# Kernel optimization log

Measured on AMD Instinct MI355X. Metric: run time of the kernel, lower is better.

Reference implementation:

```python
import jax, jax.numpy as jnp
import numpy as np

IN_FEATURES = 4096
OUT_FEATURES = 16384
BATCH = 2
SEQ = 2048


def setup_inputs() -> dict:
    key = jax.random.key(0)
    k_x, k_s, k_sgn, k_b = jax.random.split(key, 4)
    x = jax.random.normal(k_x, (BATCH, SEQ, IN_FEATURES), dtype=jnp.float32)
    # stored: uint8-style inverse-log magnitudes in [1, 255]
    stored = jax.random.randint(k_s, (OUT_FEATURES, IN_FEATURES), 1, 256, dtype=jnp.int32)
    # sign in {0,1}; mapped to {-1,+1} inside reference
    sign = jax.random.randint(k_sgn, (OUT_FEATURES, IN_FEATURES), 0, 2, dtype=jnp.int32)
    # log range matching typical weight magnitudes exp(-8)..exp(0)
    log_min = jnp.full((1,), -8.0, dtype=jnp.float32)
    log_max = jnp.full((1,), 0.0, dtype=jnp.float32)
    bias = jax.random.normal(k_b, (OUT_FEATURES,), dtype=jnp.float32) * 0.02
    return {"x": x, "stored": stored, "sign": sign, "log_min": log_min,
            "log_max": log_max, "bias": bias}


def _dequant_qins(stored, sign, log_min, log_max):
    # reverse inverse mapping: stored in [1,255] -> normalized in [0,1]
    normalized = (255.0 - stored.astype(jnp.float32)) / 254.0
    log_weight = log_min + normalized * (log_max - log_min)
    sign_f = (2 * sign - 1).astype(jnp.float32)  # {0,1} -> {-1,+1}
    return sign_f * jnp.exp(log_weight)  # [out, in] fp32


def reference(x, stored, sign, log_min, log_max, bias):
    lmin = log_min[0]
    lmax = log_max[0]
    w = _dequant_qins(stored, sign, lmin, lmax)  # [O, I]
    # F.linear: y = x @ w.T + bias
    out = jnp.einsum('bsi,oi->bso', x, w) + bias
    return out
```

## Files before the change

### kernel.cpp

```cpp
#include <hip/hip_runtime.h>
#include <stdint.h>

#define M_DIM 4096
#define N_DIM 16384
#define K_DIM 4096
#define BM 256
#define BN 256
#define BK 64
#define NT (K_DIM / BK)

typedef __attribute__((ext_vector_type(8))) __bf16 bf16x8;
typedef __attribute__((ext_vector_type(4))) float f32x4;

__device__ __forceinline__ unsigned short f2bf(float f) {
    uint32_t u = __builtin_bit_cast(uint32_t, f);
    uint32_t r = (u + 0x7FFFu + ((u >> 16) & 1u)) >> 16;
    return (unsigned short)r;
}

union Pack8 { unsigned short h[8]; uint4 v; };

__device__ __forceinline__ void async_copy16(const void* g, void* l) {
    __builtin_amdgcn_global_load_lds((__attribute__((address_space(1))) void*)(g),
                                     (__attribute__((address_space(3))) void*)(l),
                                     16, 0, 0);
}

#define BARRIER() do { asm volatile("" ::: "memory"); \
                       __builtin_amdgcn_s_barrier();  \
                       asm volatile("" ::: "memory"); } while (0)

__global__ __launch_bounds__(256) void cast_x_kernel(const float* __restrict__ x,
                                                     unsigned short* __restrict__ xb,
                                                     int n8) {
    for (int i = blockIdx.x * blockDim.x + threadIdx.x; i < n8;
         i += gridDim.x * blockDim.x) {
        const float4* p = (const float4*)(x + (size_t)i * 8);
        float4 v0 = p[0], v1 = p[1];
        Pack8 o;
        o.h[0] = f2bf(v0.x); o.h[1] = f2bf(v0.y);
        o.h[2] = f2bf(v0.z); o.h[3] = f2bf(v0.w);
        o.h[4] = f2bf(v1.x); o.h[5] = f2bf(v1.y);
        o.h[6] = f2bf(v1.z); o.h[7] = f2bf(v1.w);
        *(uint4*)(xb + (size_t)i * 8) = o.v;
    }
}

__global__ __launch_bounds__(256) void dequant_kernel(const int* __restrict__ stored,
                                                      const int* __restrict__ sign,
                                                      const float* __restrict__ log_min,
                                                      const float* __restrict__ log_max,
                                                      unsigned short* __restrict__ wb,
                                                      int n8) {
    const float lmin = log_min[0];
    const float lrange = log_max[0] - lmin;
    for (int i = blockIdx.x * blockDim.x + threadIdx.x; i < n8;
         i += gridDim.x * blockDim.x) {
        const int4* ps = (const int4*)(stored + (size_t)i * 8);
        const int4* pg = (const int4*)(sign + (size_t)i * 8);
        int4 s0 = ps[0], s1 = ps[1];
        int4 g0 = pg[0], g1 = pg[1];
        int sv[8] = {s0.x, s0.y, s0.z, s0.w, s1.x, s1.y, s1.z, s1.w};
        int gv[8] = {g0.x, g0.y, g0.z, g0.w, g1.x, g1.y, g1.z, g1.w};
        Pack8 o;
#pragma unroll
        for (int j = 0; j < 8; ++j) {
            float nrm = (255.0f - (float)sv[j]) * (1.0f / 254.0f);
            float w = __expf(lmin + nrm * lrange);
            o.h[j] = f2bf(gv[j] ? w : -w);
        }
        *(uint4*)(wb + (size_t)i * 8) = o.v;
    }
}

__global__ __launch_bounds__(512, 1) void gemm_kernel(const unsigned short* __restrict__ A,
                                                      const unsigned short* __restrict__ W,
                                                      const float* __restrict__ bias,
                                                      float* __restrict__ C) {
    extern __shared__ char lds[];
    const int tid  = threadIdx.x;
    const int wave = tid >> 6;
    const int lane = tid & 63;
    const int l15  = lane & 15;
    const int l16  = lane >> 4;
    const int wr   = wave >> 2;
    const int wc   = wave & 3;

    const int bid = blockIdx.x;
    const int wg  = ((bid & 7) << 7) | (bid >> 3);
    const int rowBase = (wg >> 6) * BM;
    const int colBase = (wg & 63) * BN;

    f32x4 acc[8][4] = {};

    auto stage_half = [&](int t, int d, int u) {
        const int kb = t * BK;
        const unsigned short* g = (u < 2) ? A : W;
        const int rb = ((u < 2) ? rowBase : colBase) + (u & 1) * 128;
        char* hb = lds + d * 65536 + ((u < 2) ? 0 : 32768) + (u & 1) * 16384;
#pragma unroll
        for (int sub = 0; sub < 2; ++sub) {
            const int Ld   = (sub * 512 + tid) * 16;
            const int r    = Ld >> 7;
            const int colb = (Ld & 127) ^ ((r & 7) << 4);
            async_copy16(g + (size_t)(rb + r) * K_DIM + kb + (colb >> 1),
                         hb + (sub * 512 + wave * 64) * 16);
        }
    };

    stage_half(0, 0, 0); stage_half(0, 0, 1);
    stage_half(0, 0, 2); stage_half(0, 0, 3);
    stage_half(1, 1, 0); stage_half(1, 1, 1);

    for (int t = 0; t < NT; ++t) {
        const int c = t & 1;
        if (t + 1 < NT) asm volatile("s_waitcnt vmcnt(4)" ::: "memory");
        else            asm volatile("s_waitcnt vmcnt(0)" ::: "memory");
        BARRIER();
        __builtin_amdgcn_sched_barrier(0);

        const char* bA  = lds + c * 65536 + wr * 16384;
        const char* bB  = lds + c * 65536 + 32768 + (wc >> 1) * 16384;
        const int   brB = (wc & 1) * 64;

        bf16x8 aF[4][2];
        bf16x8 bF[2][2];
#pragma unroll
        for (int q = 0; q < 4; ++q) {
            const int mq = q >> 1, nq = q & 1;
            if (nq == 0) {
#pragma unroll
                for (int i = 0; i < 4; ++i)
#pragma unroll
                    for (int ks = 0; ks < 2; ++ks) {
                        const int r    = (mq * 4 + i) * 16 + l15;
                        const int colb = (ks * 64 + l16 * 16) ^ ((r & 7) << 4);
                        aF[i][ks] = *(const bf16x8*)(bA + (r << 7) + colb);
                    }
            }
#pragma unroll
            for (int j = 0; j < 2; ++j)
#pragma unroll
                for (int ks = 0; ks < 2; ++ks) {
                    const int r    = brB + (nq * 2 + j) * 16 + l15;
                    const int colb = (ks * 64 + l16 * 16) ^ ((r & 7) << 4);
                    bF[j][ks] = *(const bf16x8*)(bB + (r << 7) + colb);
                }
            if (q == 0 && t + 1 < NT) stage_half(t + 1, c ^ 1, 2);
            if (q == 1 && t + 1 < NT) stage_half(t + 1, c ^ 1, 3);
            if (q == 3 && t + 2 < NT) {
                stage_half(t + 2, c, 0);
                stage_half(t + 2, c, 1);
            }
            BARRIER();
            asm volatile("s_waitcnt lgkmcnt(0)" ::: "memory");
            __builtin_amdgcn_sched_barrier(0);
            __builtin_amdgcn_s_setprio(1);
#pragma unroll
            for (int i = 0; i < 4; ++i)
#pragma unroll
                for (int j = 0; j < 2; ++j)
#pragma unroll
                    for (int ks = 0; ks < 2; ++ks)
                        acc[mq * 4 + i][nq * 2 + j] =
                            __builtin_amdgcn_mfma_f32_16x16x32_bf16(
                                aF[i][ks], bF[j][ks], acc[mq * 4 + i][nq * 2 + j],
                                0, 0, 0);
            __builtin_amdgcn_s_setprio(0);
            BARRIER();
        }
    }

#pragma unroll
    for (int m = 0; m < 8; ++m) {
        const int grow0 = rowBase + wr * 128 + m * 16 + l16 * 4;
#pragma unroll
        for (int n = 0; n < 4; ++n) {
            const int gcol = colBase + wc * 64 + n * 16 + l15;
            const float bv = bias[gcol];
#pragma unroll
            for (int r4 = 0; r4 < 4; ++r4)
                C[(size_t)(grow0 + r4) * N_DIM + gcol] = acc[m][n][r4] + bv;
        }
    }
}

extern "C" void kernel_launch(void* const* d_in, const int* in_sizes, int n_in,
                              void* d_out, int out_size, void* d_ws, size_t ws_size,
                              hipStream_t stream) {
    const float* x       = (const float*)d_in[0];
    const int*   stored  = (const int*)d_in[1];
    const int*   sign    = (const int*)d_in[2];
    const float* log_min = (const float*)d_in[3];
    const float* log_max = (const float*)d_in[4];
    const float* bias    = (const float*)d_in[5];
    float* out = (float*)d_out;

    unsigned short* Ab = (unsigned short*)d_ws;
    unsigned short* Wb = (unsigned short*)((char*)d_ws +
                          (size_t)M_DIM * K_DIM * sizeof(unsigned short));

    cast_x_kernel<<<2048, 256, 0, stream>>>(x, Ab, (M_DIM * K_DIM) / 8);
    dequant_kernel<<<4096, 256, 0, stream>>>(stored, sign, log_min, log_max, Wb,
                                             (N_DIM * K_DIM) / 8);

    hipFuncSetAttribute((const void*)gemm_kernel,
                        hipFuncAttributeMaxDynamicSharedMemorySize, 131072);
    gemm_kernel<<<dim3((M_DIM / BM) * (N_DIM / BN)), dim3(512), 131072, stream>>>(
        Ab, Wb, bias, out);
}
```

Measured before the change: 654.1 us.

## Shrink GEMM tiles to 128x128 with simpler double-buffered pipeline

Halves the block tile from 256x256 to 128x128, so there are four times as many workgroups, with 64 KB of LDS each. The launch bound now asks for four blocks per CU instead of one. The staged quarter-pipeline is replaced by a plain double buffer: the next K tile is prefetched once per iteration and each wave computes a 64x32 sub-tile. The aim is more occupancy and simpler synchronisation. The cost is less operand reuse per loaded byte, a higher ratio of LDS reads to MFMAs, and more global and L2 traffic.

```diff
diff --git a/kernel.cpp b/kernel.cpp
--- a/kernel.cpp
+++ b/kernel.cpp
@@ -4,8 +4,8 @@
 #define M_DIM 4096
 #define N_DIM 16384
 #define K_DIM 4096
-#define BM 256
-#define BN 256
+#define BM 128
+#define BN 128
 #define BK 64
 #define NT (K_DIM / BK)
 
@@ -73,7 +73,7 @@
     }
 }
 
-__global__ __launch_bounds__(512, 1) void gemm_kernel(const unsigned short* __restrict__ A,
+__global__ __launch_bounds__(512, 4) void gemm_kernel(const unsigned short* __restrict__ A,
                                                       const unsigned short* __restrict__ W,
                                                       const float* __restrict__ bias,
                                                       float* __restrict__ C) {
@@ -87,17 +87,17 @@
     const int wc   = wave & 3;
 
     const int bid = blockIdx.x;
-    const int wg  = ((bid & 7) << 7) | (bid >> 3);
-    const int rowBase = (wg >> 6) * BM;
-    const int colBase = (wg & 63) * BN;
+    const int wg  = ((bid & 7) << 9) | (bid >> 3);
+    const int rowBase = (wg >> 7) * BM;
+    const int colBase = (wg & 127) * BN;
 
-    f32x4 acc[8][4] = {};
+    f32x4 acc[4][2] = {};
 
-    auto stage_half = [&](int t, int d, int u) {
+    auto stage = [&](int t, int u) {
         const int kb = t * BK;
-        const unsigned short* g = (u < 2) ? A : W;
-        const int rb = ((u < 2) ? rowBase : colBase) + (u & 1) * 128;
-        char* hb = lds + d * 65536 + ((u < 2) ? 0 : 32768) + (u & 1) * 16384;
+        const unsigned short* g = u ? W : A;
+        const int rb = u ? colBase : rowBase;
+        char* hb = lds + ((t & 1) << 15) + (u << 14);
 #pragma unroll
         for (int sub = 0; sub < 2; ++sub) {
             const int Ld   = (sub * 512 + tid) * 16;
@@ -108,75 +108,63 @@
         }
     };
 
-    stage_half(0, 0, 0); stage_half(0, 0, 1);
-    stage_half(0, 0, 2); stage_half(0, 0, 3);
-    stage_half(1, 1, 0); stage_half(1, 1, 1);
+    stage(0, 0); stage(0, 1);
 
     for (int t = 0; t < NT; ++t) {
         const int c = t & 1;
-        if (t + 1 < NT) asm volatile("s_waitcnt vmcnt(4)" ::: "memory");
-        else            asm volatile("s_waitcnt vmcnt(0)" ::: "memory");
+        if (t + 1 < NT) {
+            stage(t + 1, 0);
+            asm volatile("s_waitcnt vmcnt(2)" ::: "memory");
+        } else {
+            asm volatile("s_waitcnt vmcnt(0)" ::: "memory");
+        }
         BARRIER();
         __builtin_amdgcn_sched_barrier(0);
 
-        const char* bA  = lds + c * 65536 + wr * 16384;
-        const char* bB  = lds + c * 65536 + 32768 + (wc >> 1) * 16384;
-        const int   brB = (wc & 1) * 64;
+        const char* bA = lds + (c << 15);
+        const char* bB = lds + (c << 15) + 16384;
 
-        bf16x8 aF[4][2];
-        bf16x8 bF[2][2];
+        bf16x8 aF[4][2], bF[2][2];
 #pragma unroll
-        for (int q = 0; q < 4; ++q) {
-            const int mq = q >> 1, nq = q & 1;
-            if (nq == 0) {
+        for (int m = 0; m < 4; ++m)
 #pragma unroll
-                for (int i = 0; i < 4; ++i)
-#pragma unroll
-                    for (int ks = 0; ks < 2; ++ks) {
-                        const int r    = (mq * 4 + i) * 16 + l15;
-                        const int colb = (ks * 64 + l16 * 16) ^ ((r & 7) << 4);
-                        aF[i][ks] = *(const bf16x8*)(bA + (r << 7) + colb);
-                    }
+            for (int ks = 0; ks < 2; ++ks) {
+                const int r    = wr * 64 + m * 16 + l15;
+                const int colb = (ks * 64 + l16 * 16) ^ ((r & 7) << 4);
+                aF[m][ks] = *(const bf16x8*)(bA + (r << 7) + colb);
             }
 #pragma unroll
-            for (int j = 0; j < 2; ++j)
+        for (int n = 0; n < 2; ++n)
 #pragma unroll
-                for (int ks = 0; ks < 2; ++ks) {
-                    const int r    = brB + (nq * 2 + j) * 16 + l15;
-                    const int colb = (ks * 64 + l16 * 16) ^ ((r & 7) << 4);
-                    bF[j][ks] = *(const bf16x8*)(bB + (r << 7) + colb);
-                }
-            if (q == 0 && t + 1 < NT) stage_half(t + 1, c ^ 1, 2);
-            if (q == 1 && t + 1 < NT) stage_half(t + 1, c ^ 1, 3);
-            if (q == 3 && t + 2 < NT) {
-                stage_half(t + 2, c, 0);
-                stage_half(t + 2, c, 1);
+            for (int ks = 0; ks < 2; ++ks) {
+                const int r    = wc * 32 + n * 16 + l15;
+                const int colb = (ks * 64 + l16 * 16) ^ ((r & 7) << 4);
+                bF[n][ks] = *(const bf16x8*)(bB + (r << 7) + colb);
             }
-            BARRIER();
-            asm volatile("s_waitcnt lgkmcnt(0)" ::: "memory");
-            __builtin_amdgcn_sched_barrier(0);
-            __builtin_amdgcn_s_setprio(1);
+        if (t + 1 < NT) stage(t + 1, 1);
+        asm volatile("s_waitcnt lgkmcnt(8)" ::: "memory");
+        BARRIER();
+        asm volatile("s_waitcnt lgkmcnt(0)" ::: "memory");
+        __builtin_amdgcn_sched_barrier(0);
+        __builtin_amdgcn_s_setprio(1);
 #pragma unroll
-            for (int i = 0; i < 4; ++i)
+        for (int m = 0; m < 4; ++m)
 #pragma unroll
-                for (int j = 0; j < 2; ++j)
+            for (int n = 0; n < 2; ++n)
 #pragma unroll
-                    for (int ks = 0; ks < 2; ++ks)
-                        acc[mq * 4 + i][nq * 2 + j] =
-                            __builtin_amdgcn_mfma_f32_16x16x32_bf16(
-                                aF[i][ks], bF[j][ks], acc[mq * 4 + i][nq * 2 + j],
-                                0, 0, 0);
-            __builtin_amdgcn_s_setprio(0);
-            BARRIER();
-        }
+                for (int ks = 0; ks < 2; ++ks)
+                    acc[m][n] = __builtin_amdgcn_mfma_f32_16x16x32_bf16(
+                        aF[m][ks], bF[n][ks], acc[m][n], 0, 0, 0);
+        __builtin_amdgcn_s_setprio(0);
+        BARRIER();
     }
 
 #pragma unroll
-    for (int m = 0; m < 8; ++m) {
-        const int grow0 = rowBase + wr * 128 + m * 16 + l16 * 4;
+    for (int m = 0; m < 4; ++m) {
+        const int grow0 = rowBase + wr * 64 + m * 16 + l16 * 4;
 #pragma unroll
-        for (int n = 0; n < 4; ++n) {
-            const int gcol = colBase + wc * 64 + n * 16 + l15;
+        for (int n = 0; n < 2; ++n) {
+            const int gcol = colBase + wc * 32 + n * 16 + l15;
             const float bv = bias[gcol];
 #pragma unroll
             for (int r4 = 0; r4 < 4; ++r4)
@@ -205,7 +193,7 @@
                                              (N_DIM * K_DIM) / 8);
 
     hipFuncSetAttribute((const void*)gemm_kernel,
-                        hipFuncAttributeMaxDynamicSharedMemorySize, 131072);
-    gemm_kernel<<<dim3((M_DIM / BM) * (N_DIM / BN)), dim3(512), 131072, stream>>>(
+                        hipFuncAttributeMaxDynamicSharedMemorySize, 65536);
+    gemm_kernel<<<dim3((M_DIM / BM) * (N_DIM / BN)), dim3(512), 65536, stream>>>(
         Ab, Wb, bias, out);
 }
```

Result: slower. 783.1 us (+19.7%).

## Restructure GEMM main loop into four MFMA phases with fewer barriers

Applied to the files above, without the earlier changes.

Replaces the four-quadrant inner loop, which used two barriers per quadrant, with a flatter schedule. Both B fragment halves and the first A half are loaded up front, the second A half is loaded mid-iteration, and only one barrier remains before the t+2 prefetch. Global-to-LDS prefetches are interleaved between the MFMA blocks to cut synchronisation overhead. It also raises launch bounds to request two blocks per CU. That caps registers well below what the 128 accumulators plus all live A/B fragments need, so spills are a serious risk, and the 128 KB LDS allocation may not allow a second block anyway.

```diff
diff --git a/kernel.cpp b/kernel.cpp
--- a/kernel.cpp
+++ b/kernel.cpp
@@ -73,7 +73,7 @@
     }
 }
 
-__global__ __launch_bounds__(512, 1) void gemm_kernel(const unsigned short* __restrict__ A,
+__global__ __launch_bounds__(512, 2) void gemm_kernel(const unsigned short* __restrict__ A,
                                                       const unsigned short* __restrict__ W,
                                                       const float* __restrict__ bias,
                                                       float* __restrict__ C) {
@@ -117,58 +117,92 @@
         if (t + 1 < NT) asm volatile("s_waitcnt vmcnt(4)" ::: "memory");
         else            asm volatile("s_waitcnt vmcnt(0)" ::: "memory");
         BARRIER();
-        __builtin_amdgcn_sched_barrier(0);
 
         const char* bA  = lds + c * 65536 + wr * 16384;
         const char* bB  = lds + c * 65536 + 32768 + (wc >> 1) * 16384;
         const int   brB = (wc & 1) * 64;
 
-        bf16x8 aF[4][2];
-        bf16x8 bF[2][2];
-#pragma unroll
-        for (int q = 0; q < 4; ++q) {
-            const int mq = q >> 1, nq = q & 1;
-            if (nq == 0) {
-#pragma unroll
-                for (int i = 0; i < 4; ++i)
-#pragma unroll
-                    for (int ks = 0; ks < 2; ++ks) {
-                        const int r    = (mq * 4 + i) * 16 + l15;
-                        const int colb = (ks * 64 + l16 * 16) ^ ((r & 7) << 4);
-                        aF[i][ks] = *(const bf16x8*)(bA + (r << 7) + colb);
-                    }
-            }
-#pragma unroll
-            for (int j = 0; j < 2; ++j)
-#pragma unroll
-                for (int ks = 0; ks < 2; ++ks) {
-                    const int r    = brB + (nq * 2 + j) * 16 + l15;
-                    const int colb = (ks * 64 + l16 * 16) ^ ((r & 7) << 4);
-                    bF[j][ks] = *(const bf16x8*)(bB + (r << 7) + colb);
-                }
-            if (q == 0 && t + 1 < NT) stage_half(t + 1, c ^ 1, 2);
-            if (q == 1 && t + 1 < NT) stage_half(t + 1, c ^ 1, 3);
-            if (q == 3 && t + 2 < NT) {
-                stage_half(t + 2, c, 0);
-                stage_half(t + 2, c, 1);
-            }
-            BARRIER();
-            asm volatile("s_waitcnt lgkmcnt(0)" ::: "memory");
-            __builtin_amdgcn_sched_barrier(0);
-            __builtin_amdgcn_s_setprio(1);
-#pragma unroll
-            for (int i = 0; i < 4; ++i)
-#pragma unroll
-                for (int j = 0; j < 2; ++j)
-#pragma unroll
-                    for (int ks = 0; ks < 2; ++ks)
-                        acc[mq * 4 + i][nq * 2 + j] =
-                            __builtin_amdgcn_mfma_f32_16x16x32_bf16(
-                                aF[i][ks], bF[j][ks], acc[mq * 4 + i][nq * 2 + j],
-                                0, 0, 0);
-            __builtin_amdgcn_s_setprio(0);
-            BARRIER();
-        }
+        bf16x8 aF0[4][2], aF1[4][2], bF0[2][2], bF1[2][2];
+
+#pragma unroll
+        for (int i = 0; i < 4; ++i)
+#pragma unroll
+            for (int ks = 0; ks < 2; ++ks) {
+                const int r    = i * 16 + l15;
+                const int colb = (ks * 64 + l16 * 16) ^ ((r & 7) << 4);
+                aF0[i][ks] = *(const bf16x8*)(bA + (r << 7) + colb);
+            }
+#pragma unroll
+        for (int j = 0; j < 2; ++j)
+#pragma unroll
+            for (int ks = 0; ks < 2; ++ks) {
+                const int r    = brB + j * 16 + l15;
+                const int colb = (ks * 64 + l16 * 16) ^ ((r & 7) << 4);
+                bF0[j][ks] = *(const bf16x8*)(bB + (r << 7) + colb);
+            }
+#pragma unroll
+        for (int j = 0; j < 2; ++j)
+#pragma unroll
+            for (int ks = 0; ks < 2; ++ks) {
+                const int r    = brB + 32 + j * 16 + l15;
+                const int colb = (ks * 64 + l16 * 16) ^ ((r & 7) << 4);
+                bF1[j][ks] = *(const bf16x8*)(bB + (r << 7) + colb);
+            }
+        if (t + 1 < NT) stage_half(t + 1, c ^ 1, 2);
+        __builtin_amdgcn_s_setprio(1);
+#pragma unroll
+        for (int i = 0; i < 4; ++i)
+#pragma unroll
+            for (int j = 0; j < 2; ++j)
+#pragma unroll
+                for (int ks = 0; ks < 2; ++ks)
+                    acc[i][j] = __builtin_amdgcn_mfma_f32_16x16x32_bf16(
+                        aF0[i][ks], bF0[j][ks], acc[i][j], 0, 0, 0);
+        __builtin_amdgcn_s_setprio(0);
+
+#pragma unroll
+        for (int i = 0; i < 4; ++i)
+#pragma unroll
+            for (int ks = 0; ks < 2; ++ks) {
+                const int r    = 64 + i * 16 + l15;
+                const int colb = (ks * 64 + l16 * 16) ^ ((r & 7) << 4);
+                aF1[i][ks] = *(const bf16x8*)(bA + (r << 7) + colb);
+            }
+        if (t + 1 < NT) stage_half(t + 1, c ^ 1, 3);
+        __builtin_amdgcn_s_setprio(1);
+#pragma unroll
+        for (int i = 0; i < 4; ++i)
+#pragma unroll
+            for (int j = 0; j < 2; ++j)
+#pragma unroll
+                for (int ks = 0; ks < 2; ++ks)
+                    acc[i][2 + j] = __builtin_amdgcn_mfma_f32_16x16x32_bf16(
+                        aF0[i][ks], bF1[j][ks], acc[i][2 + j], 0, 0, 0);
+        __builtin_amdgcn_s_setprio(0);
+
+        __builtin_amdgcn_s_setprio(1);
+#pragma unroll
+        for (int i = 0; i < 4; ++i)
+#pragma unroll
+            for (int j = 0; j < 2; ++j)
+#pragma unroll
+                for (int ks = 0; ks < 2; ++ks)
+                    acc[4 + i][j] = __builtin_amdgcn_mfma_f32_16x16x32_bf16(
+                        aF1[i][ks], bF0[j][ks], acc[4 + i][j], 0, 0, 0);
+        __builtin_amdgcn_s_setprio(0);
+        BARRIER();
+
+        if (t + 2 < NT) { stage_half(t + 2, c, 0); stage_half(t + 2, c, 1); }
+        __builtin_amdgcn_s_setprio(1);
+#pragma unroll
+        for (int i = 0; i < 4; ++i)
+#pragma unroll
+            for (int j = 0; j < 2; ++j)
+#pragma unroll
+                for (int ks = 0; ks < 2; ++ks)
+                    acc[4 + i][2 + j] = __builtin_amdgcn_mfma_f32_16x16x32_bf16(
+                        aF1[i][ks], bF1[j][ks], acc[4 + i][2 + j], 0, 0, 0);
+        __builtin_amdgcn_s_setprio(0);
     }
 
 #pragma unroll
```

Result: faster. 617.9 us (median of 3 runs) (-5.5%).
